# Kernel optimization log

Hardware: AMD Instinct MI355X
Metric: run time of the kernel (lower is better)

Reference implementation:

```python
import jax, jax.numpy as jnp
import numpy as np

HEADS = 8
DIM_HEAD = 64
QUERY_DIM = 512
CONTEXT_DIM = 512
OUT_DIM = 512
INNER = HEADS * DIM_HEAD  # 512


def setup_inputs() -> dict:
    key = jax.random.key(0)
    ks = jax.random.split(key, 6)
    B, N, S, M = 2, 1024, 4, 2048
    x = jax.random.normal(ks[0], (B, N, S, QUERY_DIM), dtype=jnp.float32)
    context = jax.random.normal(ks[1], (B, M, CONTEXT_DIM), dtype=jnp.float32)
    # Linear weights stored as [in, out] so y = x @ W (matches torch Linear with W.T)
    Wq = jax.random.normal(ks[2], (QUERY_DIM, INNER), dtype=jnp.float32) / np.sqrt(QUERY_DIM)
    Wkv = jax.random.normal(ks[3], (CONTEXT_DIM, 2 * INNER), dtype=jnp.float32) / np.sqrt(CONTEXT_DIM)
    Wo = jax.random.normal(ks[4], (INNER, OUT_DIM), dtype=jnp.float32) / np.sqrt(INNER)
    bo = jax.random.normal(ks[5], (OUT_DIM,), dtype=jnp.float32) * 0.01
    return {"x": x, "context": context, "Wq": Wq, "Wkv": Wkv, "Wo": Wo, "bo": bo}


def reference(x, context, Wq, Wkv, Wo, bo):
    B, N, S, _ = x.shape
    M = context.shape[1]
    scale = DIM_HEAD ** -0.5
    # projections
    q = (x @ Wq).reshape(B, N, S, HEADS, DIM_HEAD)            # b n s h d
    kv = context @ Wkv                                        # b m (2*inner)
    k, v = jnp.split(kv, 2, axis=-1)
    k = k.reshape(B, M, HEADS, DIM_HEAD)                      # b m h d
    v = v.reshape(B, M, HEADS, DIM_HEAD)
    # attention scores: [(b h) s n m] expressed as bhsnm
    sim = jnp.einsum('bnshd,bmhd->bhsnm', q, k) * scale
    attn = jax.nn.softmax(sim, axis=-1)
    out = jnp.einsum('bhsnm,bmhd->bnshd', attn, v)            # b n s h d
    out = out.reshape(B, N, S, INNER)
    return out @ Wo + bo
```

## Files before the change

### kernel.cpp

```cpp
#include <hip/hip_runtime.h>

typedef __bf16 bf16;
typedef __bf16 bf16x8 __attribute__((ext_vector_type(8)));
typedef __bf16 bf16x4 __attribute__((ext_vector_type(4)));
typedef float f32x4 __attribute__((ext_vector_type(4)));

#define SCL 0.18033688011112042f

#define GLOAD_LDS16(g, l)                                          \
  __builtin_amdgcn_global_load_lds(                                \
      (const __attribute__((address_space(1))) void*)(g),          \
      (__attribute__((address_space(3))) void*)(l), 16, 0, 0)

static __device__ __forceinline__ unsigned pk_bf16(float a, float b) {
  union { bf16 h[2]; unsigned u; } cv;
  cv.h[0] = (bf16)a; cv.h[1] = (bf16)b;
  return cv.u;
}
static __device__ __forceinline__ void pl32swap(unsigned& a, unsigned& b) {
  auto r = __builtin_amdgcn_permlane32_swap(a, b, false, false);
  a = r[0]; b = r[1];
}
static __device__ __forceinline__ void pl16swap(unsigned& a, unsigned& b) {
  auto r = __builtin_amdgcn_permlane16_swap(a, b, false, false);
  a = r[0]; b = r[1];
}

__global__ __launch_bounds__(256) void prep_kernel(const float* __restrict__ x,
                                                   const float* __restrict__ ctx,
                                                   const float* __restrict__ Wq,
                                                   const float* __restrict__ Wkv,
                                                   const float* __restrict__ Wo,
                                                   bf16* __restrict__ xb,
                                                   bf16* __restrict__ cb,
                                                   bf16* __restrict__ Wqt,
                                                   bf16* __restrict__ Wkvt,
                                                   bf16* __restrict__ Wot) {
  const int bid = blockIdx.x;
  const int tid = threadIdx.x;
  if (bid < 3072) {
    const float* src;
    bf16* dst;
    size_t off;
    if (bid < 2048) { src = x; dst = xb; off = (size_t)bid * 2048; }
    else            { src = ctx; dst = cb; off = (size_t)(bid - 2048) * 2048; }
    size_t i = off + (size_t)tid * 8;
    float4 a0 = *(const float4*)&src[i];
    float4 a1 = *(const float4*)&src[i + 4];
    bf16x8 o;
    o[0] = (bf16)a0.x; o[1] = (bf16)a0.y; o[2] = (bf16)a0.z; o[3] = (bf16)a0.w;
    o[4] = (bf16)a1.x; o[5] = (bf16)a1.y; o[6] = (bf16)a1.z; o[7] = (bf16)a1.w;
    *(bf16x8*)&dst[i] = o;
  } else {
    __shared__ float tile[32][33];
    const int idx = bid - 3072;
    const int bx = idx & 63;
    const int k0 = (idx >> 6) * 32;
    const float* W; bf16* Wt; int N, n0;
    if (bx < 16)      { W = Wq;  Wt = Wqt;  N = 512;  n0 = bx * 32; }
    else if (bx < 48) { W = Wkv; Wt = Wkvt; N = 1024; n0 = (bx - 16) * 32; }
    else              { W = Wo;  Wt = Wot;  N = 512;  n0 = (bx - 48) * 32; }
    const int j = tid & 31, i0 = tid >> 5;
#pragma unroll
    for (int ii = 0; ii < 4; ii++) {
      int i = i0 * 4 + ii;
      tile[i][j] = W[(size_t)(k0 + i) * N + n0 + j];
    }
    __syncthreads();
#pragma unroll
    for (int ii = 0; ii < 4; ii++) {
      int i = i0 * 4 + ii;
      Wt[(size_t)(n0 + i) * 512 + k0 + j] = (bf16)tile[j][i];
    }
  }
}

__device__ __forceinline__ void gemm128x64_core(const bf16* __restrict__ A,
                                                const bf16* __restrict__ Bt,
                                                int m0, int n0,
                                                bf16* As, bf16* Bs,
                                                f32x4 (&acc)[4][2],
                                                int wave, int lane) {
  const int l15 = lane & 15, quad = lane >> 4;
  const int psw = l15 & 7;
  const int lrow = lane >> 3;
  const int gchunk = (lane & 7) ^ lrow;
  const bf16* Ag = A + (size_t)(m0 + wave * 32 + lrow) * 512 + gchunk * 8;
  const bf16* Bg = Bt + (size_t)(n0 + wave * 16 + lrow) * 512 + gchunk * 8;
  bf16* Asw = As + wave * 32 * 64;
  bf16* Bsw = Bs + wave * 16 * 64;
  const int wm = (wave >> 1) * 64, wn = (wave & 1) * 32;

#pragma unroll
  for (int g = 0; g < 4; g++)
    GLOAD_LDS16(Ag + (size_t)(g * 8) * 512, Asw + g * 8 * 64);
#pragma unroll
  for (int g = 0; g < 2; g++)
    GLOAD_LDS16(Bg + (size_t)(g * 8) * 512, Bsw + g * 8 * 64);
  __syncthreads();

  for (int t = 0; t < 8; t++) {
    if (t < 7) {
      const int kt = (t + 1) * 64;
      const int nb = (t + 1) & 1;
#pragma unroll
      for (int g = 0; g < 4; g++)
        GLOAD_LDS16(Ag + kt + (size_t)(g * 8) * 512, Asw + nb * (128 * 64) + g * 8 * 64);
#pragma unroll
      for (int g = 0; g < 2; g++)
        GLOAD_LDS16(Bg + kt + (size_t)(g * 8) * 512, Bsw + nb * (64 * 64) + g * 8 * 64);
    }
    const bf16* Ac = As + (t & 1) * (128 * 64);
    const bf16* Bc = Bs + (t & 1) * (64 * 64);
#pragma unroll
    for (int h = 0; h < 2; h++) {
      bf16x8 af[4], bfr[2];
#pragma unroll
      for (int i = 0; i < 4; i++)
        af[i] = *(const bf16x8*)&Ac[(wm + i * 16 + l15) * 64 + (((h * 4 + quad) ^ psw) * 8)];
#pragma unroll
      for (int j = 0; j < 2; j++)
        bfr[j] = *(const bf16x8*)&Bc[(wn + j * 16 + l15) * 64 + (((h * 4 + quad) ^ psw) * 8)];
#pragma unroll
      for (int i = 0; i < 4; i++)
#pragma unroll
        for (int j = 0; j < 2; j++)
          acc[i][j] = __builtin_amdgcn_mfma_f32_16x16x32_bf16(af[i], bfr[j], acc[i][j], 0, 0, 0);
    }
    __syncthreads();
  }
}

__device__ __forceinline__ void gemm128x128_core(const bf16* __restrict__ A,
                                                 const bf16* __restrict__ Bt,
                                                 int m0, int n0,
                                                 bf16* As, bf16* Bs,
                                                 f32x4 (&acc)[4][4],
                                                 int wave, int lane) {
  const int l15 = lane & 15, quad = lane >> 4;
  const int psw = l15 & 7;
  const int lrow = lane >> 3;
  const int gchunk = (lane & 7) ^ lrow;
  const bf16* Ag = A + (size_t)(m0 + wave * 32 + lrow) * 512 + gchunk * 8;
  const bf16* Bg = Bt + (size_t)(n0 + wave * 32 + lrow) * 512 + gchunk * 8;
  bf16* Asw = As + wave * 32 * 64;
  bf16* Bsw = Bs + wave * 32 * 64;
  const int wm = (wave >> 1) * 64, wn = (wave & 1) * 64;

#pragma unroll
  for (int g = 0; g < 4; g++) {
    GLOAD_LDS16(Ag + (size_t)(g * 8) * 512, Asw + g * 8 * 64);
    GLOAD_LDS16(Bg + (size_t)(g * 8) * 512, Bsw + g * 8 * 64);
  }
  __syncthreads();

  for (int t = 0; t < 8; t++) {
    if (t < 7) {
      const int kt = (t + 1) * 64;
      const int nb = (t + 1) & 1;
#pragma unroll
      for (int g = 0; g < 4; g++) {
        GLOAD_LDS16(Ag + kt + (size_t)(g * 8) * 512, Asw + nb * (128 * 64) + g * 8 * 64);
        GLOAD_LDS16(Bg + kt + (size_t)(g * 8) * 512, Bsw + nb * (128 * 64) + g * 8 * 64);
      }
    }
    const bf16* Ac = As + (t & 1) * (128 * 64);
    const bf16* Bc = Bs + (t & 1) * (128 * 64);
#pragma unroll
    for (int h = 0; h < 2; h++) {
      bf16x8 af[4], bfr[4];
#pragma unroll
      for (int i = 0; i < 4; i++)
        af[i] = *(const bf16x8*)&Ac[(wm + i * 16 + l15) * 64 + (((h * 4 + quad) ^ psw) * 8)];
#pragma unroll
      for (int j = 0; j < 4; j++)
        bfr[j] = *(const bf16x8*)&Bc[(wn + j * 16 + l15) * 64 + (((h * 4 + quad) ^ psw) * 8)];
#pragma unroll
      for (int i = 0; i < 4; i++)
#pragma unroll
        for (int j = 0; j < 4; j++)
          acc[i][j] = __builtin_amdgcn_mfma_f32_16x16x32_bf16(af[i], bfr[j], acc[i][j], 0, 0, 0);
    }
    __syncthreads();
  }
}

__global__ __launch_bounds__(256, 2) void proj_kernel(const bf16* __restrict__ xb,
                                                      const bf16* __restrict__ cb,
                                                      const bf16* __restrict__ Wqt,
                                                      const bf16* __restrict__ Wkvt,
                                                      bf16* __restrict__ qb,
                                                      bf16* __restrict__ Kb,
                                                      bf16* __restrict__ Vtb) {
  __shared__ __align__(16) bf16 As[2 * 128 * 64];
  __shared__ __align__(16) bf16 Bs[2 * 128 * 64];
  const int tid = threadIdx.x;
  const int wave = tid >> 6, lane = tid & 63;
  const int quad = lane >> 4, l15 = lane & 15;
  const int bid = blockIdx.x;
  f32x4 acc[4][4] = {};
  const int wm = (wave >> 1) * 64, wn = (wave & 1) * 64;

  if (bid < 256) {
    const int m0 = (bid & 63) * 128, n0 = (bid >> 6) * 128;
    gemm128x128_core(xb, Wqt, m0, n0, As, Bs, acc, wave, lane);
#pragma unroll
    for (int i = 0; i < 4; i++) {
      const int rowb = m0 + wm + i * 16 + quad * 4;
#pragma unroll
      for (int j = 0; j < 4; j++) {
        const int col = n0 + wn + j * 16 + l15;
#pragma unroll
        for (int r = 0; r < 4; r++)
          qb[(size_t)(rowb + r) * 512 + col] = (bf16)(acc[i][j][r] * SCL);
      }
    }
  } else {
    const int idx = bid - 256;
    const int m0 = (idx & 31) * 128, n0 = (idx >> 5) * 128;
    gemm128x128_core(cb, Wkvt, m0, n0, As, Bs, acc, wave, lane);
#pragma unroll
    for (int i = 0; i < 4; i++) {
      const int rowb = m0 + wm + i * 16 + quad * 4;
#pragma unroll
      for (int j = 0; j < 4; j++) {
        const int col = n0 + wn + j * 16 + l15;
        if (col < 512) {
#pragma unroll
          for (int r = 0; r < 4; r++)
            Kb[(size_t)(rowb + r) * 512 + col] = (bf16)acc[i][j][r];
        } else {
          const int hh = (col - 512) >> 6, d = (col - 512) & 63;
          const int bb = rowb >> 11, mb = rowb & 2047;
          bf16x4 pk;
          pk[0] = (bf16)acc[i][j][0]; pk[1] = (bf16)acc[i][j][1];
          pk[2] = (bf16)acc[i][j][2]; pk[3] = (bf16)acc[i][j][3];
          *(bf16x4*)&Vtb[((size_t)(bb * 8 + hh) * 64 + d) * 2048 + mb] = pk;
        }
      }
    }
  }
}

__global__ __launch_bounds__(256, 2) void outproj_kernel(const bf16* __restrict__ attn,
                                                         const bf16* __restrict__ Wot,
                                                         float* __restrict__ out,
                                                         const float* __restrict__ bias) {
  __shared__ __align__(16) bf16 As[2 * 128 * 64];
  __shared__ __align__(16) bf16 Bs[2 * 64 * 64];
  const int tid = threadIdx.x;
  const int wave = tid >> 6, lane = tid & 63;
  const int quad = lane >> 4, l15 = lane & 15;
  const int bid = blockIdx.x;
  const int m0 = (bid & 63) * 128, n0 = (bid >> 6) * 64;
  f32x4 acc[4][2] = {};
  gemm128x64_core(attn, Wot, m0, n0, As, Bs, acc, wave, lane);
  const int wm = (wave >> 1) * 64, wn = (wave & 1) * 32;
#pragma unroll
  for (int i = 0; i < 4; i++) {
    const int rowb = m0 + wm + i * 16 + quad * 4;
#pragma unroll
    for (int j = 0; j < 2; j++) {
      const int col = n0 + wn + j * 16 + l15;
      const float bv = bias[col];
#pragma unroll
      for (int r = 0; r < 4; r++)
        out[(size_t)(rowb + r) * 512 + col] = acc[i][j][r] + bv;
    }
  }
}

__global__ __launch_bounds__(256, 2) void attn_kernel(const bf16* __restrict__ q,
                                                      const bf16* __restrict__ Kb,
                                                      const bf16* __restrict__ Vtb,
                                                      bf16* __restrict__ attn_out) {
  const int tid = threadIdx.x;
  const int wave = tid >> 6, lane = tid & 63;
  const int quad = lane >> 4, l15 = lane & 15;
  const int bid = blockIdx.x;
  const int g = bid & 15, inner = bid >> 4;
  const int b = g >> 3, h = g & 7;
  const int s = inner & 3, nt = inner >> 2;
  const int n0 = nt * 128;

  __shared__ __align__(16) bf16 Kl[2][64 * 64];
  __shared__ __align__(16) bf16 Vl[2][64 * 64];

  size_t qoff[2];
  bf16x8 qf[2][2];
#pragma unroll
  for (int cg = 0; cg < 2; cg++) {
    const int n = n0 + wave * 32 + cg * 16 + l15;
    qoff[cg] = ((size_t)((b * 1024 + n) * 4 + s)) * 512 + h * 64;
    qf[cg][0] = *(const bf16x8*)&q[qoff[cg] + quad * 8];
    qf[cg][1] = *(const bf16x8*)&q[qoff[cg] + 32 + quad * 8];
  }

  f32x4 o[2][4] = {};
  f32x4 ol[2] = {};
  bf16x8 ones;
#pragma unroll
  for (int i = 0; i < 8; i++) ones[i] = (bf16)1.0f;

  const int srow = tid >> 2, c0 = tid & 3;
  const bf16* Kg = Kb + (size_t)(b * 2048 + srow) * 512 + h * 64 + c0 * 16;
  const bf16* Vg = Vtb + ((size_t)(b * 8 + h) * 64 + srow) * 2048 + c0 * 16;
  const int ssw = srow & 7;
  const int koff0 = srow * 64 + ((c0 * 2) ^ ssw) * 8;
  const int koff1 = srow * 64 + ((c0 * 2 + 1) ^ ssw) * 8;

  uint4 kr0 = *(const uint4*)Kg;
  uint4 kr1 = *(const uint4*)(Kg + 8);
  uint4 vr0 = *(const uint4*)Vg;
  uint4 vr1 = *(const uint4*)(Vg + 8);
  *(uint4*)&Kl[0][koff0] = kr0; *(uint4*)&Kl[0][koff1] = kr1;
  *(uint4*)&Vl[0][koff0] = vr0; *(uint4*)&Vl[0][koff1] = vr1;

  const int psw = l15 & 7;

  for (int t = 0; t < 32; ++t) {
    __syncthreads();
    if (t < 31) {
      const bf16* kg = Kg + (size_t)(t + 1) * 64 * 512;
      const bf16* vg = Vg + (t + 1) * 64;
      kr0 = *(const uint4*)kg; kr1 = *(const uint4*)(kg + 8);
      vr0 = *(const uint4*)vg; vr1 = *(const uint4*)(vg + 8);
    }
    const bf16* Kc = &Kl[t & 1][0];
    const bf16* Vc = &Vl[t & 1][0];

    __builtin_amdgcn_s_setprio(1);

    f32x4 sf[2][4];
#pragma unroll
    for (int mc = 0; mc < 4; mc++) {
      bf16x8 kf0 = *(const bf16x8*)&Kc[(mc * 16 + l15) * 64 + ((quad ^ psw) * 8)];
      bf16x8 kf1 = *(const bf16x8*)&Kc[(mc * 16 + l15) * 64 + (((4 + quad) ^ psw) * 8)];
#pragma unroll
      for (int cg = 0; cg < 2; cg++) {
        f32x4 z = {};
        z = __builtin_amdgcn_mfma_f32_16x16x32_bf16(kf0, qf[cg][0], z, 0, 0, 0);
        z = __builtin_amdgcn_mfma_f32_16x16x32_bf16(kf1, qf[cg][1], z, 0, 0, 0);
        sf[cg][mc] = z;
      }
    }

    unsigned w[2][4][2];
#pragma unroll
    for (int cg = 0; cg < 2; cg++)
#pragma unroll
      for (int mc = 0; mc < 4; mc++) {
        const float e0 = __builtin_amdgcn_exp2f(sf[cg][mc][0]);
        const float e1 = __builtin_amdgcn_exp2f(sf[cg][mc][1]);
        const float e2 = __builtin_amdgcn_exp2f(sf[cg][mc][2]);
        const float e3 = __builtin_amdgcn_exp2f(sf[cg][mc][3]);
        w[cg][mc][0] = pk_bf16(e0, e1);
        w[cg][mc][1] = pk_bf16(e2, e3);
      }

    bf16x8 pf[2][2];
#pragma unroll
    for (int cg = 0; cg < 2; cg++)
#pragma unroll
      for (int mch = 0; mch < 2; mch++) {
        unsigned tw0, tw1, tw2, tw3;
        {
          unsigned a = w[cg][2 * mch][0], bb2 = w[cg][2 * mch + 1][0];
          pl32swap(a, bb2);
          pl16swap(a, bb2);
          tw0 = a; tw2 = bb2;
        }
        {
          unsigned a = w[cg][2 * mch][1], bb2 = w[cg][2 * mch + 1][1];
          pl32swap(a, bb2);
          pl16swap(a, bb2);
          tw1 = a; tw3 = bb2;
        }
        union { unsigned u[4]; bf16x8 v; } cv;
        cv.u[0] = tw0; cv.u[1] = tw1; cv.u[2] = tw2; cv.u[3] = tw3;
        pf[mch][cg] = cv.v;
      }

#pragma unroll
    for (int mch = 0; mch < 2; mch++) {
#pragma unroll
      for (int dg = 0; dg < 4; dg++) {
        bf16x8 vf = *(const bf16x8*)&Vc[(dg * 16 + l15) * 64 + (((mch * 4 + quad) ^ psw)) * 8];
#pragma unroll
        for (int cg = 0; cg < 2; cg++)
          o[cg][dg] = __builtin_amdgcn_mfma_f32_16x16x32_bf16(vf, pf[mch][cg], o[cg][dg], 0, 0, 0);
      }
#pragma unroll
      for (int cg = 0; cg < 2; cg++)
        ol[cg] = __builtin_amdgcn_mfma_f32_16x16x32_bf16(ones, pf[mch][cg], ol[cg], 0, 0, 0);
    }

    __builtin_amdgcn_s_setprio(0);

    if (t < 31) {
      bf16* Kn = &Kl[(t + 1) & 1][0];
      bf16* Vn = &Vl[(t + 1) & 1][0];
      *(uint4*)&Kn[koff0] = kr0; *(uint4*)&Kn[koff1] = kr1;
      *(uint4*)&Vn[koff0] = vr0; *(uint4*)&Vn[koff1] = vr1;
    }
  }

#pragma unroll
  for (int cg = 0; cg < 2; cg++) {
    const float inv = 1.0f / ol[cg][0];
#pragma unroll
    for (int dg = 0; dg < 4; dg++) {
      bf16x4 ok;
      ok[0] = (bf16)(o[cg][dg][0] * inv); ok[1] = (bf16)(o[cg][dg][1] * inv);
      ok[2] = (bf16)(o[cg][dg][2] * inv); ok[3] = (bf16)(o[cg][dg][3] * inv);
      *(bf16x4*)&attn_out[qoff[cg] + dg * 16 + quad * 4] = ok;
    }
  }
}

extern "C" void kernel_launch(void* const* d_in, const int* in_sizes, int n_in,
                              void* d_out, int out_size, void* d_ws, size_t ws_size,
                              hipStream_t stream) {
  const float* x = (const float*)d_in[0];
  const float* context = (const float*)d_in[1];
  const float* Wq = (const float*)d_in[2];
  const float* Wkv = (const float*)d_in[3];
  const float* Wo = (const float*)d_in[4];
  const float* bo = (const float*)d_in[5];
  float* out = (float*)d_out;

  char* ws = (char*)d_ws;
  bf16* xb   = (bf16*)(ws);
  bf16* cb   = (bf16*)(ws + (8u << 20));
  bf16* qb   = (bf16*)(ws + (12u << 20));
  bf16* Kb   = (bf16*)(ws + (20u << 20));
  bf16* Vtb  = (bf16*)(ws + (24u << 20));
  bf16* Wqt  = (bf16*)(ws + (28u << 20));
  bf16* Wkvt = (bf16*)(ws + (28u << 20) + 524288);
  bf16* Wot  = (bf16*)(ws + (28u << 20) + 1572864);
  bf16* attn = xb;

  prep_kernel<<<4096, 256, 0, stream>>>(x, context, Wq, Wkv, Wo, xb, cb, Wqt, Wkvt, Wot);
  proj_kernel<<<512, 256, 0, stream>>>(xb, cb, Wqt, Wkvt, qb, Kb, Vtb);
  attn_kernel<<<512, 256, 0, stream>>>(qb, Kb, Vtb, attn);
  outproj_kernel<<<512, 256, 0, stream>>>(attn, Wot, out, bo);
}
```

Before: 150.9 us.

## Fuse four stages into one cooperative persistent kernel with grid syncs

```diff
diff --git a/kernel.cpp b/kernel.cpp
--- a/kernel.cpp
+++ b/kernel.cpp
@@ -1,4 +1,7 @@
 #include <hip/hip_runtime.h>
+#include <hip/hip_cooperative_groups.h>
+
+namespace cg = cooperative_groups;
 
 typedef __bf16 bf16;
 typedef __bf16 bf16x8 __attribute__((ext_vector_type(8)));
@@ -24,55 +27,6 @@
 static __device__ __forceinline__ void pl16swap(unsigned& a, unsigned& b) {
   auto r = __builtin_amdgcn_permlane16_swap(a, b, false, false);
   a = r[0]; b = r[1];
-}
-
-__global__ __launch_bounds__(256) void prep_kernel(const float* __restrict__ x,
-                                                   const float* __restrict__ ctx,
-                                                   const float* __restrict__ Wq,
-                                                   const float* __restrict__ Wkv,
-                                                   const float* __restrict__ Wo,
-                                                   bf16* __restrict__ xb,
-                                                   bf16* __restrict__ cb,
-                                                   bf16* __restrict__ Wqt,
-                                                   bf16* __restrict__ Wkvt,
-                                                   bf16* __restrict__ Wot) {
-  const int bid = blockIdx.x;
-  const int tid = threadIdx.x;
-  if (bid < 3072) {
-    const float* src;
-    bf16* dst;
-    size_t off;
-    if (bid < 2048) { src = x; dst = xb; off = (size_t)bid * 2048; }
-    else            { src = ctx; dst = cb; off = (size_t)(bid - 2048) * 2048; }
-    size_t i = off + (size_t)tid * 8;
-    float4 a0 = *(const float4*)&src[i];
-    float4 a1 = *(const float4*)&src[i + 4];
-    bf16x8 o;
-    o[0] = (bf16)a0.x; o[1] = (bf16)a0.y; o[2] = (bf16)a0.z; o[3] = (bf16)a0.w;
-    o[4] = (bf16)a1.x; o[5] = (bf16)a1.y; o[6] = (bf16)a1.z; o[7] = (bf16)a1.w;
-    *(bf16x8*)&dst[i] = o;
-  } else {
-    __shared__ float tile[32][33];
-    const int idx = bid - 3072;
-    const int bx = idx & 63;
-    const int k0 = (idx >> 6) * 32;
-    const float* W; bf16* Wt; int N, n0;
-    if (bx < 16)      { W = Wq;  Wt = Wqt;  N = 512;  n0 = bx * 32; }
-    else if (bx < 48) { W = Wkv; Wt = Wkvt; N = 1024; n0 = (bx - 16) * 32; }
-    else              { W = Wo;  Wt = Wot;  N = 512;  n0 = (bx - 48) * 32; }
-    const int j = tid & 31, i0 = tid >> 5;
-#pragma unroll
-    for (int ii = 0; ii < 4; ii++) {
-      int i = i0 * 4 + ii;
-      tile[i][j] = W[(size_t)(k0 + i) * N + n0 + j];
-    }
-    __syncthreads();
-#pragma unroll
-    for (int ii = 0; ii < 4; ii++) {
-      int i = i0 * 4 + ii;
-      Wt[(size_t)(n0 + i) * 512 + k0 + j] = (bf16)tile[j][i];
-    }
-  }
 }
 
 __device__ __forceinline__ void gemm128x64_core(const bf16* __restrict__ A,
@@ -185,19 +139,65 @@
   }
 }
 
-__global__ __launch_bounds__(256, 2) void proj_kernel(const bf16* __restrict__ xb,
-                                                      const bf16* __restrict__ cb,
-                                                      const bf16* __restrict__ Wqt,
-                                                      const bf16* __restrict__ Wkvt,
-                                                      bf16* __restrict__ qb,
-                                                      bf16* __restrict__ Kb,
-                                                      bf16* __restrict__ Vtb) {
-  __shared__ __align__(16) bf16 As[2 * 128 * 64];
-  __shared__ __align__(16) bf16 Bs[2 * 128 * 64];
-  const int tid = threadIdx.x;
+__device__ __forceinline__ void prep_body(int bid, int tid, char* smem,
+                                          const float* x, const float* ctx,
+                                          const float* Wq, const float* Wkv,
+                                          const float* Wo,
+                                          bf16* xb, bf16* cb,
+                                          bf16* Wqt, bf16* Wkvt, bf16* Wot) {
+#pragma unroll
+  for (int k = 0; k < 4; k++) {
+    size_t i = ((size_t)bid * 4 + k) * 2048 + (size_t)tid * 8;
+    float4 a0 = *(const float4*)&x[i];
+    float4 a1 = *(const float4*)&x[i + 4];
+    bf16x8 o;
+    o[0] = (bf16)a0.x; o[1] = (bf16)a0.y; o[2] = (bf16)a0.z; o[3] = (bf16)a0.w;
+    o[4] = (bf16)a1.x; o[5] = (bf16)a1.y; o[6] = (bf16)a1.z; o[7] = (bf16)a1.w;
+    *(bf16x8*)&xb[i] = o;
+  }
+#pragma unroll
+  for (int k = 0; k < 2; k++) {
+    size_t i = ((size_t)bid * 2 + k) * 2048 + (size_t)tid * 8;
+    float4 a0 = *(const float4*)&ctx[i];
+    float4 a1 = *(const float4*)&ctx[i + 4];
+    bf16x8 o;
+    o[0] = (bf16)a0.x; o[1] = (bf16)a0.y; o[2] = (bf16)a0.z; o[3] = (bf16)a0.w;
+    o[4] = (bf16)a1.x; o[5] = (bf16)a1.y; o[6] = (bf16)a1.z; o[7] = (bf16)a1.w;
+    *(bf16x8*)&cb[i] = o;
+  }
+  float (*tile)[33] = (float(*)[33])smem;
+  const int j = tid & 31, i0 = tid >> 5;
+  for (int k = 0; k < 2; k++) {
+    const int idx = bid * 2 + k;
+    const int bx = idx & 63;
+    const int k0 = (idx >> 6) * 32;
+    const float* W; bf16* Wt; int N, n0;
+    if (bx < 16)      { W = Wq;  Wt = Wqt;  N = 512;  n0 = bx * 32; }
+    else if (bx < 48) { W = Wkv; Wt = Wkvt; N = 1024; n0 = (bx - 16) * 32; }
+    else              { W = Wo;  Wt = Wot;  N = 512;  n0 = (bx - 48) * 32; }
+    __syncthreads();
+#pragma unroll
+    for (int ii = 0; ii < 4; ii++) {
+      int i = i0 * 4 + ii;
+      tile[i][j] = W[(size_t)(k0 + i) * N + n0 + j];
+    }
+    __syncthreads();
+#pragma unroll
+    for (int ii = 0; ii < 4; ii++) {
+      int i = i0 * 4 + ii;
+      Wt[(size_t)(n0 + i) * 512 + k0 + j] = (bf16)tile[j][i];
+    }
+  }
+}
+
+__device__ __forceinline__ void proj_body(int bid, int tid, char* smem,
+                                          const bf16* xb, const bf16* cb,
+                                          const bf16* Wqt, const bf16* Wkvt,
+                                          bf16* qb, bf16* Kb, bf16* Vtb) {
+  bf16* As = (bf16*)smem;
+  bf16* Bs = As + 2 * 128 * 64;
   const int wave = tid >> 6, lane = tid & 63;
   const int quad = lane >> 4, l15 = lane & 15;
-  const int bid = blockIdx.x;
   f32x4 acc[4][4] = {};
   const int wm = (wave >> 1) * 64, wn = (wave & 1) * 64;
 
@@ -242,58 +242,27 @@
   }
 }
 
-__global__ __launch_bounds__(256, 2) void outproj_kernel(const bf16* __restrict__ attn,
-                                                         const bf16* __restrict__ Wot,
-                                                         float* __restrict__ out,
-                                                         const float* __restrict__ bias) {
-  __shared__ __align__(16) bf16 As[2 * 128 * 64];
-  __shared__ __align__(16) bf16 Bs[2 * 64 * 64];
-  const int tid = threadIdx.x;
+__device__ __forceinline__ void attn_body(int bid, int tid, char* smem,
+                                          const bf16* q, const bf16* Kb,
+                                          const bf16* Vtb, bf16* attn_out) {
   const int wave = tid >> 6, lane = tid & 63;
   const int quad = lane >> 4, l15 = lane & 15;
-  const int bid = blockIdx.x;
-  const int m0 = (bid & 63) * 128, n0 = (bid >> 6) * 64;
-  f32x4 acc[4][2] = {};
-  gemm128x64_core(attn, Wot, m0, n0, As, Bs, acc, wave, lane);
-  const int wm = (wave >> 1) * 64, wn = (wave & 1) * 32;
-#pragma unroll
-  for (int i = 0; i < 4; i++) {
-    const int rowb = m0 + wm + i * 16 + quad * 4;
-#pragma unroll
-    for (int j = 0; j < 2; j++) {
-      const int col = n0 + wn + j * 16 + l15;
-      const float bv = bias[col];
-#pragma unroll
-      for (int r = 0; r < 4; r++)
-        out[(size_t)(rowb + r) * 512 + col] = acc[i][j][r] + bv;
-    }
-  }
-}
-
-__global__ __launch_bounds__(256, 2) void attn_kernel(const bf16* __restrict__ q,
-                                                      const bf16* __restrict__ Kb,
-                                                      const bf16* __restrict__ Vtb,
-                                                      bf16* __restrict__ attn_out) {
-  const int tid = threadIdx.x;
-  const int wave = tid >> 6, lane = tid & 63;
-  const int quad = lane >> 4, l15 = lane & 15;
-  const int bid = blockIdx.x;
   const int g = bid & 15, inner = bid >> 4;
   const int b = g >> 3, h = g & 7;
   const int s = inner & 3, nt = inner >> 2;
   const int n0 = nt * 128;
 
-  __shared__ __align__(16) bf16 Kl[2][64 * 64];
-  __shared__ __align__(16) bf16 Vl[2][64 * 64];
+  bf16* Kl0 = (bf16*)smem;
+  bf16* Vl0 = Kl0 + 2 * 64 * 64;
 
   size_t qoff[2];
   bf16x8 qf[2][2];
 #pragma unroll
-  for (int cg = 0; cg < 2; cg++) {
-    const int n = n0 + wave * 32 + cg * 16 + l15;
-    qoff[cg] = ((size_t)((b * 1024 + n) * 4 + s)) * 512 + h * 64;
-    qf[cg][0] = *(const bf16x8*)&q[qoff[cg] + quad * 8];
-    qf[cg][1] = *(const bf16x8*)&q[qoff[cg] + 32 + quad * 8];
+  for (int cg2 = 0; cg2 < 2; cg2++) {
+    const int n = n0 + wave * 32 + cg2 * 16 + l15;
+    qoff[cg2] = ((size_t)((b * 1024 + n) * 4 + s)) * 512 + h * 64;
+    qf[cg2][0] = *(const bf16x8*)&q[qoff[cg2] + quad * 8];
+    qf[cg2][1] = *(const bf16x8*)&q[qoff[cg2] + 32 + quad * 8];
   }
 
   f32x4 o[2][4] = {};
@@ -313,8 +282,9 @@
   uint4 kr1 = *(const uint4*)(Kg + 8);
   uint4 vr0 = *(const uint4*)Vg;
   uint4 vr1 = *(const uint4*)(Vg + 8);
-  *(uint4*)&Kl[0][koff0] = kr0; *(uint4*)&Kl[0][koff1] = kr1;
-  *(uint4*)&Vl[0][koff0] = vr0; *(uint4*)&Vl[0][koff1] = vr1;
+  __syncthreads();
+  *(uint4*)&Kl0[koff0] = kr0; *(uint4*)&Kl0[koff1] = kr1;
+  *(uint4*)&Vl0[koff0] = vr0; *(uint4*)&Vl0[koff1] = vr1;
 
   const int psw = l15 & 7;
 
@@ -326,8 +296,8 @@
       kr0 = *(const uint4*)kg; kr1 = *(const uint4*)(kg + 8);
       vr0 = *(const uint4*)vg; vr1 = *(const uint4*)(vg + 8);
     }
-    const bf16* Kc = &Kl[t & 1][0];
-    const bf16* Vc = &Vl[t & 1][0];
+    const bf16* Kc = Kl0 + (t & 1) * (64 * 64);
+    const bf16* Vc = Vl0 + (t & 1) * (64 * 64);
 
     __builtin_amdgcn_s_setprio(1);
 
@@ -337,48 +307,48 @@
       bf16x8 kf0 = *(const bf16x8*)&Kc[(mc * 16 + l15) * 64 + ((quad ^ psw) * 8)];
       bf16x8 kf1 = *(const bf16x8*)&Kc[(mc * 16 + l15) * 64 + (((4 + quad) ^ psw) * 8)];
 #pragma unroll
-      for (int cg = 0; cg < 2; cg++) {
+      for (int cg2 = 0; cg2 < 2; cg2++) {
         f32x4 z = {};
-        z = __builtin_amdgcn_mfma_f32_16x16x32_bf16(kf0, qf[cg][0], z, 0, 0, 0);
-        z = __builtin_amdgcn_mfma_f32_16x16x32_bf16(kf1, qf[cg][1], z, 0, 0, 0);
-        sf[cg][mc] = z;
+        z = __builtin_amdgcn_mfma_f32_16x16x32_bf16(kf0, qf[cg2][0], z, 0, 0, 0);
+        z = __builtin_amdgcn_mfma_f32_16x16x32_bf16(kf1, qf[cg2][1], z, 0, 0, 0);
+        sf[cg2][mc] = z;
       }
     }
 
     unsigned w[2][4][2];
 #pragma unroll
-    for (int cg = 0; cg < 2; cg++)
+    for (int cg2 = 0; cg2 < 2; cg2++)
 #pragma unroll
       for (int mc = 0; mc < 4; mc++) {
-        const float e0 = __builtin_amdgcn_exp2f(sf[cg][mc][0]);
-        const float e1 = __builtin_amdgcn_exp2f(sf[cg][mc][1]);
-        const float e2 = __builtin_amdgcn_exp2f(sf[cg][mc][2]);
-        const float e3 = __builtin_amdgcn_exp2f(sf[cg][mc][3]);
-        w[cg][mc][0] = pk_bf16(e0, e1);
-        w[cg][mc][1] = pk_bf16(e2, e3);
+        const float e0 = __builtin_amdgcn_exp2f(sf[cg2][mc][0]);
+        const float e1 = __builtin_amdgcn_exp2f(sf[cg2][mc][1]);
+        const float e2 = __builtin_amdgcn_exp2f(sf[cg2][mc][2]);
+        const float e3 = __builtin_amdgcn_exp2f(sf[cg2][mc][3]);
+        w[cg2][mc][0] = pk_bf16(e0, e1);
+        w[cg2][mc][1] = pk_bf16(e2, e3);
       }
 
     bf16x8 pf[2][2];
 #pragma unroll
-    for (int cg = 0; cg < 2; cg++)
+    for (int cg2 = 0; cg2 < 2; cg2++)
 #pragma unroll
       for (int mch = 0; mch < 2; mch++) {
         unsigned tw0, tw1, tw2, tw3;
         {
-          unsigned a = w[cg][2 * mch][0], bb2 = w[cg][2 * mch + 1][0];
+          unsigned a = w[cg2][2 * mch][0], bb2 = w[cg2][2 * mch + 1][0];
           pl32swap(a, bb2);
           pl16swap(a, bb2);
           tw0 = a; tw2 = bb2;
         }
         {
-          unsigned a = w[cg][2 * mch][1], bb2 = w[cg][2 * mch + 1][1];
+          unsigned a = w[cg2][2 * mch][1], bb2 = w[cg2][2 * mch + 1][1];
           pl32swap(a, bb2);
           pl16swap(a, bb2);
           tw1 = a; tw3 = bb2;
         }
         union { unsigned u[4]; bf16x8 v; } cv;
         cv.u[0] = tw0; cv.u[1] = tw1; cv.u[2] = tw2; cv.u[3] = tw3;
-        pf[mch][cg] = cv.v;
+        pf[mch][cg2] = cv.v;
       }
 
 #pragma unroll
@@ -387,35 +357,132 @@
       for (int dg = 0; dg < 4; dg++) {
         bf16x8 vf = *(const bf16x8*)&Vc[(dg * 16 + l15) * 64 + (((mch * 4 + quad) ^ psw)) * 8];
 #pragma unroll
-        for (int cg = 0; cg < 2; cg++)
-          o[cg][dg] = __builtin_amdgcn_mfma_f32_16x16x32_bf16(vf, pf[mch][cg], o[cg][dg], 0, 0, 0);
-      }
-#pragma unroll
-      for (int cg = 0; cg < 2; cg++)
-        ol[cg] = __builtin_amdgcn_mfma_f32_16x16x32_bf16(ones, pf[mch][cg], ol[cg], 0, 0, 0);
+        for (int cg2 = 0; cg2 < 2; cg2++)
+          o[cg2][dg] = __builtin_amdgcn_mfma_f32_16x16x32_bf16(vf, pf[mch][cg2], o[cg2][dg], 0, 0, 0);
+      }
+#pragma unroll
+      for (int cg2 = 0; cg2 < 2; cg2++)
+        ol[cg2] = __builtin_amdgcn_mfma_f32_16x16x32_bf16(ones, pf[mch][cg2], ol[cg2], 0, 0, 0);
     }
 
     __builtin_amdgcn_s_setprio(0);
 
     if (t < 31) {
-      bf16* Kn = &Kl[(t + 1) & 1][0];
-      bf16* Vn = &Vl[(t + 1) & 1][0];
+      bf16* Kn = Kl0 + ((t + 1) & 1) * (64 * 64);
+      bf16* Vn = Vl0 + ((t + 1) & 1) * (64 * 64);
       *(uint4*)&Kn[koff0] = kr0; *(uint4*)&Kn[koff1] = kr1;
       *(uint4*)&Vn[koff0] = vr0; *(uint4*)&Vn[koff1] = vr1;
     }
   }
 
 #pragma unroll
-  for (int cg = 0; cg < 2; cg++) {
-    const float inv = 1.0f / ol[cg][0];
+  for (int cg2 = 0; cg2 < 2; cg2++) {
+    const float inv = 1.0f / ol[cg2][0];
 #pragma unroll
     for (int dg = 0; dg < 4; dg++) {
       bf16x4 ok;
-      ok[0] = (bf16)(o[cg][dg][0] * inv); ok[1] = (bf16)(o[cg][dg][1] * inv);
-      ok[2] = (bf16)(o[cg][dg][2] * inv); ok[3] = (bf16)(o[cg][dg][3] * inv);
-      *(bf16x4*)&attn_out[qoff[cg] + dg * 16 + quad * 4] = ok;
-    }
-  }
+      ok[0] = (bf16)(o[cg2][dg][0] * inv); ok[1] = (bf16)(o[cg2][dg][1] * inv);
+      ok[2] = (bf16)(o[cg2][dg][2] * inv); ok[3] = (bf16)(o[cg2][dg][3] * inv);
+      *(bf16x4*)&attn_out[qoff[cg2] + dg * 16 + quad * 4] = ok;
+    }
+  }
+}
+
+__device__ __forceinline__ void outproj_body(int bid, int tid, char* smem,
+                                             const bf16* attn, const bf16* Wot,
+                                             float* out, const float* bias) {
+  bf16* As = (bf16*)smem;
+  bf16* Bs = As + 2 * 128 * 64;
+  const int wave = tid >> 6, lane = tid & 63;
+  const int quad = lane >> 4, l15 = lane & 15;
+  const int m0 = (bid & 63) * 128, n0 = (bid >> 6) * 64;
+  f32x4 acc[4][2] = {};
+  gemm128x64_core(attn, Wot, m0, n0, As, Bs, acc, wave, lane);
+  const int wm = (wave >> 1) * 64, wn = (wave & 1) * 32;
+#pragma unroll
+  for (int i = 0; i < 4; i++) {
+    const int rowb = m0 + wm + i * 16 + quad * 4;
+#pragma unroll
+    for (int j = 0; j < 2; j++) {
+      const int col = n0 + wn + j * 16 + l15;
+      const float bv = bias[col];
+#pragma unroll
+      for (int r = 0; r < 4; r++)
+        out[(size_t)(rowb + r) * 512 + col] = acc[i][j][r] + bv;
+    }
+  }
+}
+
+__global__ __launch_bounds__(256, 2) void mega_kernel(
+    const float* __restrict__ x, const float* __restrict__ ctx,
+    const float* __restrict__ Wq, const float* __restrict__ Wkv,
+    const float* __restrict__ Wo, const float* __restrict__ bo,
+    bf16* __restrict__ xb, bf16* __restrict__ cb, bf16* __restrict__ qb,
+    bf16* __restrict__ Kb, bf16* __restrict__ Vtb,
+    bf16* __restrict__ Wqt, bf16* __restrict__ Wkvt, bf16* __restrict__ Wot,
+    float* __restrict__ out) {
+  __shared__ __align__(16) char smem[65536];
+  cg::grid_group grid = cg::this_grid();
+  const int tid = threadIdx.x;
+  const int bid = blockIdx.x;
+
+  prep_body(bid, tid, smem, x, ctx, Wq, Wkv, Wo, xb, cb, Wqt, Wkvt, Wot);
+  __threadfence();
+  grid.sync();
+  __threadfence();
+
+  proj_body(bid, tid, smem, xb, cb, Wqt, Wkvt, qb, Kb, Vtb);
+  __threadfence();
+  grid.sync();
+  __threadfence();
+
+  attn_body(bid, tid, smem, qb, Kb, Vtb, xb );
+  __threadfence();
+  grid.sync();
+  __threadfence();
+
+  outproj_body(bid, tid, smem, xb, Wot, out, bo);
+}
+
+__global__ __launch_bounds__(256) void prep_kernel(const float* __restrict__ x,
+                                                   const float* __restrict__ ctx,
+                                                   const float* __restrict__ Wq,
+                                                   const float* __restrict__ Wkv,
+                                                   const float* __restrict__ Wo,
+                                                   bf16* __restrict__ xb,
+                                                   bf16* __restrict__ cb,
+                                                   bf16* __restrict__ Wqt,
+                                                   bf16* __restrict__ Wkvt,
+                                                   bf16* __restrict__ Wot) {
+  __shared__ __align__(16) char smem[4352];
+  prep_body(blockIdx.x, threadIdx.x, smem, x, ctx, Wq, Wkv, Wo, xb, cb, Wqt, Wkvt, Wot);
+}
+
+__global__ __launch_bounds__(256, 2) void proj_kernel(const bf16* __restrict__ xb,
+                                                      const bf16* __restrict__ cb,
+                                                      const bf16* __restrict__ Wqt,
+                                                      const bf16* __restrict__ Wkvt,
+                                                      bf16* __restrict__ qb,
+                                                      bf16* __restrict__ Kb,
+                                                      bf16* __restrict__ Vtb) {
+  __shared__ __align__(16) char smem[65536];
+  proj_body(blockIdx.x, threadIdx.x, smem, xb, cb, Wqt, Wkvt, qb, Kb, Vtb);
+}
+
+__global__ __launch_bounds__(256, 2) void attn_kernel(const bf16* __restrict__ q,
+                                                      const bf16* __restrict__ Kb,
+                                                      const bf16* __restrict__ Vtb,
+                                                      bf16* __restrict__ attn_out) {
+  __shared__ __align__(16) char smem[32768];
+  attn_body(blockIdx.x, threadIdx.x, smem, q, Kb, Vtb, attn_out);
+}
+
+__global__ __launch_bounds__(256, 2) void outproj_kernel(const bf16* __restrict__ attn,
+                                                         const bf16* __restrict__ Wot,
+                                                         float* __restrict__ out,
+                                                         const float* __restrict__ bias) {
+  __shared__ __align__(16) char smem[49152];
+  outproj_body(blockIdx.x, threadIdx.x, smem, attn, Wot, out, bias);
 }
 
 extern "C" void kernel_launch(void* const* d_in, const int* in_sizes, int n_in,
@@ -438,10 +505,18 @@
   bf16* Wqt  = (bf16*)(ws + (28u << 20));
   bf16* Wkvt = (bf16*)(ws + (28u << 20) + 524288);
   bf16* Wot  = (bf16*)(ws + (28u << 20) + 1572864);
-  bf16* attn = xb;
-
-  prep_kernel<<<4096, 256, 0, stream>>>(x, context, Wq, Wkv, Wo, xb, cb, Wqt, Wkvt, Wot);
-  proj_kernel<<<512, 256, 0, stream>>>(xb, cb, Wqt, Wkvt, qb, Kb, Vtb);
-  attn_kernel<<<512, 256, 0, stream>>>(qb, Kb, Vtb, attn);
-  outproj_kernel<<<512, 256, 0, stream>>>(attn, Wot, out, bo);
-}
+
+  void* args[] = {(void*)&x, (void*)&context, (void*)&Wq, (void*)&Wkv,
+                  (void*)&Wo, (void*)&bo, (void*)&xb, (void*)&cb, (void*)&qb,
+                  (void*)&Kb, (void*)&Vtb, (void*)&Wqt, (void*)&Wkvt,
+                  (void*)&Wot, (void*)&out};
+  hipError_t err = hipLaunchCooperativeKernel(
+      reinterpret_cast<const void*>(mega_kernel), dim3(512), dim3(256),
+      args, 0, stream);
+  if (err != hipSuccess) {
+    prep_kernel<<<512, 256, 0, stream>>>(x, context, Wq, Wkv, Wo, xb, cb, Wqt, Wkvt, Wot);
+    proj_kernel<<<512, 256, 0, stream>>>(xb, cb, Wqt, Wkvt, qb, Kb, Vtb);
+    attn_kernel<<<512, 256, 0, stream>>>(qb, Kb, Vtb, xb);
+    outproj_kernel<<<512, 256, 0, stream>>>(xb, Wot, out, bo);
+  }
+}
```

New measurement: 596.8 us. 296% more time.
